# Kernel tuning notes

Measured on AMD Instinct MI355X. Metric: run time of the kernel, lower is better.

The kernel has to match this reference:

```python
import jax, jax.numpy as jnp
import numpy as np
from jax import lax
from jax.scipy.special import logsumexp

B, T, N = 256, 512, 128


def setup_inputs() -> dict:
    key = jax.random.key(0)
    k1, k2, k3 = jax.random.split(key, 3)
    emissions = jax.random.normal(k1, (B, T, N), dtype=jnp.float32)
    tag_ids = jax.random.randint(k2, (B, T), 0, N, dtype=jnp.int64)
    mask = jnp.ones((B, T), dtype=jnp.int32)
    # learned transition matrix (glorot-uniform-ish init)
    limit = float(np.sqrt(6.0 / (N + N)))
    trans = jax.random.uniform(k3, (N, N), minval=-limit, maxval=limit, dtype=jnp.float32)
    return {"emissions": emissions, "tag_ids": tag_ids, "mask": mask, "trans": trans}


def _sequence_score(emissions, tag_ids, maskf, trans):
    # unary: emission score of the gold tag at each valid step
    unary = jnp.take_along_axis(emissions, tag_ids[:, :, None], axis=2)[..., 0]  # [B,T]
    unary = jnp.sum(unary * maskf, axis=1)
    # binary: transition score between consecutive gold tags
    binary = trans[tag_ids[:, :-1], tag_ids[:, 1:]] * maskf[:, 1:]  # [B,T-1]
    return unary + jnp.sum(binary, axis=1)


def _log_norm(emissions, maskf, trans):
    # forward algorithm over time via lax.scan; alpha: [B,N]
    alpha0 = emissions[:, 0]
    em = jnp.swapaxes(emissions, 0, 1)[1:]   # [T-1,B,N]
    mk = jnp.swapaxes(maskf, 0, 1)[1:]       # [T-1,B]

    def step(alpha, xs):
        emit_t, m_t = xs
        new = logsumexp(alpha[:, :, None] + trans[None], axis=1) + emit_t
        alpha = jnp.where(m_t[:, None] > 0, new, alpha)
        return alpha, None

    alpha, _ = lax.scan(step, alpha0, (em, mk))
    return logsumexp(alpha, axis=1)  # [B]


def _viterbi_decode(emissions, maskf, trans):
    alpha0 = emissions[:, 0]
    em = jnp.swapaxes(emissions, 0, 1)[1:]
    mk = jnp.swapaxes(maskf, 0, 1)[1:]
    idx = jnp.arange(N, dtype=jnp.int32)[None]

    def fwd(alpha, xs):
        emit_t, m_t = xs
        scores = alpha[:, :, None] + trans[None]        # [B,N,N]
        bp = jnp.argmax(scores, axis=1).astype(jnp.int32)  # [B,N]
        new = jnp.max(scores, axis=1) + emit_t
        valid = m_t[:, None] > 0
        alpha = jnp.where(valid, new, alpha)
        bp = jnp.where(valid, bp, idx)  # carry same tag through padding
        return alpha, bp

    alpha, bps = lax.scan(fwd, alpha0, (em, mk))  # bps: [T-1,B,N]
    last_tag = jnp.argmax(alpha, axis=1).astype(jnp.int32)  # [B]

    def bwd(tag, bp_t):
        new_tag = jnp.take_along_axis(bp_t, tag[:, None], axis=1)[:, 0]
        return new_tag, new_tag

    _, tags_rev = lax.scan(bwd, last_tag, bps[::-1])  # [T-1,B]
    tags = jnp.concatenate([tags_rev[::-1], last_tag[None]], axis=0)  # [T,B]
    return jnp.swapaxes(tags, 0, 1)  # [B,T]


def reference(emissions, tag_ids, mask, trans):
    maskf = mask.astype(emissions.dtype)
    log_likelihood = _sequence_score(emissions, tag_ids, maskf, trans) - _log_norm(emissions, maskf, trans)
    predict = _viterbi_decode(emissions, maskf, trans)
    return (log_likelihood, trans, predict)
```

## Files before the change

### kernel.cpp

```cpp
#include <hip/hip_runtime.h>
#include <cmath>

#define BB 256
#define TT 512
#define NN 128
#define LN2F 0.6931471805599453f

__device__ __forceinline__ float wave_max64(float v) {
    #pragma unroll
    for (int off = 32; off; off >>= 1) v = fmaxf(v, __shfl_xor(v, off));
    return v;
}
__device__ __forceinline__ float wave_sum64(float v) {
    #pragma unroll
    for (int off = 32; off; off >>= 1) v += __shfl_xor(v, off);
    return v;
}
__device__ __forceinline__ int wave_argmax128(float v0, float v1, int l) {
    float m = fmaxf(v0, v1);
    float wm = wave_max64(m);
    unsigned long long ball = __ballot(m == wm);
    int lane = __ffsll(ball) - 1;
    int idx = (v0 == wm) ? (2 * l) : (2 * l + 1);
    return __shfl(idx, lane);
}

__device__ __forceinline__ int padidx(int i) { return 36 * (i >> 5) + (i & 31); }

__global__ __launch_bounds__(1024, 4) void fwd_kernel(
        const float* __restrict__ em, const int* __restrict__ mask,
        const float* __restrict__ trans, float* __restrict__ outp,
        float* __restrict__ lognorm) {
    const int b = blockIdx.x;
    const int tid = threadIdx.x;
    const int w = tid >> 6;
    const int l = tid & 63;
    const bool isV = (w < 8);
    const int wl = w & 7;
    const int j = (l & 15) + 16 * wl;
    const int q = l >> 4;
    const int i0 = 32 * q;

    float C[32];
    {
        const float* tc = trans + (size_t)i0 * NN + j;
        #pragma unroll
        for (int r = 0; r < 32; ++r) C[r] = tc[(size_t)r * NN];
        if (!isV) {
            #pragma unroll
            for (int r = 0; r < 32; ++r) C[r] = __expf(C[r]);
        }
    }

    __shared__ __align__(16) float apad[2][144];
    __shared__ __align__(16) float spad[2][144];
    __shared__ unsigned char bp_lds[TT * NN];
    __shared__ unsigned char tags_lds[TT];
    __shared__ int msk[TT];
    __shared__ float piv[2];
    __shared__ float sfin[NN];
    __shared__ int kacc_sh;

    if (tid < TT) msk[tid] = mask[b * TT + tid];

    const float* emb = em + (size_t)b * TT * NN;

    float e0 = emb[j];
    float st = 0.f;
    int kacc = 0;
    if (isV) {
        st = e0;
        if (l < 16) apad[0][padidx(j)] = st;
    } else {
        st = __expf(e0);
        if (l < 16) spad[0][padidx(j)] = st;
        if (w == 8 && l == 0) piv[0] = st;
    }
    float e_next = emb[NN + j];
    __syncthreads();

    for (int t = 1; t < TT; ++t) {
        const float e_cur = e_next;
        if (t + 1 < TT) e_next = emb[(size_t)(t + 1) * NN + j];
        const int m = msk[t];
        const int p = (t - 1) & 1, qb = t & 1;

        if (isV) {
            const float4* ap = (const float4*)(apad[p] + 36 * q);
            float m0 = -INFINITY, m1 = -INFINITY, m2 = -INFINITY, m3 = -INFINITY;
            int u0 = 0, u1 = 0, u2 = 0, u3 = 0;
            #pragma unroll
            for (int u = 0; u < 8; ++u) {
                float4 v = ap[u];
                float c0 = v.x + C[4*u+0];
                float c1 = v.y + C[4*u+1];
                float c2 = v.z + C[4*u+2];
                float c3 = v.w + C[4*u+3];
                if (c0 > m0) { m0 = c0; u0 = u; }
                if (c1 > m1) { m1 = c1; u1 = u; }
                if (c2 > m2) { m2 = c2; u2 = u; }
                if (c3 > m3) { m3 = c3; u3 = u; }
            }
            float bv = m0; int bi = i0 + 4 * u0;
            { int id = i0 + 4*u1 + 1; if (m1 > bv || (m1 == bv && id < bi)) { bv = m1; bi = id; } }
            { int id = i0 + 4*u2 + 2; if (m2 > bv || (m2 == bv && id < bi)) { bv = m2; bi = id; } }
            { int id = i0 + 4*u3 + 3; if (m3 > bv || (m3 == bv && id < bi)) { bv = m3; bi = id; } }
            #pragma unroll
            for (int off = 16; off <= 32; off <<= 1) {
                float ov = __shfl_xor(bv, off);
                int oi = __shfl_xor(bi, off);
                if (ov > bv || (ov == bv && oi < bi)) { bv = ov; bi = oi; }
            }
            if (l < 16) {
                float av_new; int bp;
                if (m) { av_new = bv + e_cur; bp = bi; }
                else   { av_new = st;         bp = j;  }
                st = av_new;
                apad[qb][padidx(j)] = av_new;
                bp_lds[t * NN + j] = (unsigned char)bp;
            }
        } else {
            const float pv = piv[p];
            const float4* sp = (const float4*)(spad[p] + 36 * q);
            float d0 = 0, d1 = 0, d2 = 0, d3 = 0;
            #pragma unroll
            for (int u = 0; u < 8; ++u) {
                float4 v = sp[u];
                d0 = fmaf(v.x, C[4*u+0], d0);
                d1 = fmaf(v.y, C[4*u+1], d1);
                d2 = fmaf(v.z, C[4*u+2], d2);
                d3 = fmaf(v.w, C[4*u+3], d3);
            }
            float dot = (d0 + d1) + (d2 + d3);
            dot += __shfl_xor(dot, 16);
            dot += __shfl_xor(dot, 32);
            const int k = (int)(__float_as_uint(pv) >> 23) - 127;
            const float scale = __uint_as_float((unsigned)(127 - k) << 23);
            float s_new;
            if (m) { s_new = dot * scale * __expf(e_cur); kacc += k; }
            else   { s_new = st; }
            st = s_new;
            if (l < 16) {
                spad[qb][padidx(j)] = s_new;
                if (tid == 512 + 0 && false) {}
            }
            if (w == 8 && l == 0) piv[qb] = s_new;
        }
        __syncthreads();
    }

    if (!isV && l < 16) sfin[j] = st;
    if (w == 8 && l == 0) kacc_sh = kacc;
    __syncthreads();

    if (w == 0) {
        float v = sfin[2 * l] + sfin[2 * l + 1];
        v = wave_sum64(v);
        if (l == 0) lognorm[b] = __logf(v) + (float)kacc_sh * LN2F;
    } else if (w == 1) {
        float a0 = apad[(TT - 1) & 1][padidx(2 * l)];
        float a1 = apad[(TT - 1) & 1][padidx(2 * l + 1)];
        int tag = wave_argmax128(a0, a1, l);
        if (l == 0) {
            tags_lds[TT - 1] = (unsigned char)tag;
            for (int t = TT - 1; t >= 1; --t) {
                tag = bp_lds[t * NN + tag];
                tags_lds[t - 1] = (unsigned char)tag;
            }
        }
    }
    __syncthreads();
    if (tid < TT) outp[(size_t)b * TT + tid] = (float)tags_lds[tid];
}

__global__ __launch_bounds__(128, 1) void score_kernel(
        const float* __restrict__ em, const int* __restrict__ tags,
        const int* __restrict__ mask, const float* __restrict__ trans,
        const float* __restrict__ lognorm, float* __restrict__ out_ll) {
    const int b = blockIdx.x;
    const int tid = threadIdx.x;
    float acc = 0.f;
    for (int t = tid; t < TT; t += 128) {
        int tg = tags[b * TT + t];
        float mf = (float)mask[b * TT + t];
        acc += em[((size_t)b * TT + t) * NN + tg] * mf;
        if (t >= 1) {
            int tp = tags[b * TT + t - 1];
            acc += trans[tp * NN + tg] * mf;
        }
    }
    acc = wave_sum64(acc);
    __shared__ float rs[2];
    if ((tid & 63) == 0) rs[tid >> 6] = acc;
    __syncthreads();
    if (tid == 0) out_ll[b] = (rs[0] + rs[1]) - lognorm[b];
}

__global__ void copy_trans_kernel(const float* __restrict__ trans,
                                  float* __restrict__ dst) {
    int i = blockIdx.x * 256 + threadIdx.x;
    if (i < NN * NN) dst[i] = trans[i];
}

extern "C" void kernel_launch(void* const* d_in, const int* in_sizes, int n_in,
                              void* d_out, int out_size, void* d_ws, size_t ws_size,
                              hipStream_t stream) {
    const float* em = (const float*)d_in[0];
    const int* tags = (const int*)d_in[1];
    const int* mask = (const int*)d_in[2];
    const float* trans = (const float*)d_in[3];

    float* out = (float*)d_out;
    float* out_ll = out;
    float* out_trans = out + BB;
    float* out_pred = out + BB + NN * NN;

    float* lognorm = (float*)d_ws;

    hipLaunchKernelGGL(fwd_kernel, dim3(BB), dim3(1024), 0, stream,
                       em, mask, trans, out_pred, lognorm);
    hipLaunchKernelGGL(copy_trans_kernel, dim3(64), dim3(256), 0, stream,
                       trans, out_trans);
    hipLaunchKernelGGL(score_kernel, dim3(BB), dim3(128), 0, stream,
                       em, tags, mask, trans, lognorm, out_ll);
}
```

Baseline: 585.2 us.

## Split Viterbi and forward recurrences into separate 512-thread blocks with parallel backtrace

```diff
diff --git a/kernel.cpp b/kernel.cpp
--- a/kernel.cpp
+++ b/kernel.cpp
@@ -27,17 +27,17 @@
 
 __device__ __forceinline__ int padidx(int i) { return 36 * (i >> 5) + (i & 31); }
 
-__global__ __launch_bounds__(1024, 4) void fwd_kernel(
+__global__ __launch_bounds__(512, 2) void fwd_kernel(
         const float* __restrict__ em, const int* __restrict__ mask,
         const float* __restrict__ trans, float* __restrict__ outp,
         float* __restrict__ lognorm) {
-    const int b = blockIdx.x;
+    const int bi = blockIdx.x;
+    const int b = bi >> 1;
+    const bool isV = (bi & 1) == 0;
     const int tid = threadIdx.x;
     const int w = tid >> 6;
     const int l = tid & 63;
-    const bool isV = (w < 8);
-    const int wl = w & 7;
-    const int j = (l & 15) + 16 * wl;
+    const int j = (l & 15) + 16 * w;
     const int q = l >> 4;
     const int i0 = 32 * q;
 
@@ -52,76 +52,121 @@
         }
     }
 
-    __shared__ __align__(16) float apad[2][144];
-    __shared__ __align__(16) float spad[2][144];
+    __shared__ __align__(16) float stA[144], stB[144];
     __shared__ unsigned char bp_lds[TT * NN];
     __shared__ unsigned char tags_lds[TT];
+    __shared__ unsigned char map_lds[8 * NN];
+    __shared__ int entry_sh[8];
     __shared__ int msk[TT];
     __shared__ float piv[2];
     __shared__ float sfin[NN];
-    __shared__ int kacc_sh;
-
-    if (tid < TT) msk[tid] = mask[b * TT + tid];
+    __shared__ int misc[2];
+
+    msk[tid] = mask[b * TT + tid];
 
     const float* emb = em + (size_t)b * TT * NN;
-
-    float e0 = emb[j];
     float st = 0.f;
     int kacc = 0;
-    if (isV) {
-        st = e0;
-        if (l < 16) apad[0][padidx(j)] = st;
-    } else {
-        st = __expf(e0);
-        if (l < 16) spad[0][padidx(j)] = st;
-        if (w == 8 && l == 0) piv[0] = st;
+    {
+        float a0 = emb[j];
+        if (isV) {
+            st = a0;
+            if (l < 16) stA[padidx(j)] = a0;
+        } else {
+            st = __expf(a0);
+            if (l < 16) stA[padidx(j)] = st;
+            if (tid == 0) piv[0] = st;
+        }
     }
     float e_next = emb[NN + j];
     __syncthreads();
 
-    for (int t = 1; t < TT; ++t) {
-        const float e_cur = e_next;
-        if (t + 1 < TT) e_next = emb[(size_t)(t + 1) * NN + j];
-        const int m = msk[t];
-        const int p = (t - 1) & 1, qb = t & 1;
-
-        if (isV) {
-            const float4* ap = (const float4*)(apad[p] + 36 * q);
+    if (isV) {
+        const float4* apA = (const float4*)(stA + 36 * q);
+        const float4* apB = (const float4*)(stB + 36 * q);
+
+        auto VSTEP = [&](int t, const float4* ap, float* dst) {
+            const float e_cur = e_next;
+            if (t + 1 < TT) e_next = emb[(size_t)(t + 1) * NN + j];
+            const int m = msk[t];
             float m0 = -INFINITY, m1 = -INFINITY, m2 = -INFINITY, m3 = -INFINITY;
             int u0 = 0, u1 = 0, u2 = 0, u3 = 0;
             #pragma unroll
             for (int u = 0; u < 8; ++u) {
                 float4 v = ap[u];
-                float c0 = v.x + C[4*u+0];
-                float c1 = v.y + C[4*u+1];
-                float c2 = v.z + C[4*u+2];
-                float c3 = v.w + C[4*u+3];
-                if (c0 > m0) { m0 = c0; u0 = u; }
-                if (c1 > m1) { m1 = c1; u1 = u; }
-                if (c2 > m2) { m2 = c2; u2 = u; }
-                if (c3 > m3) { m3 = c3; u3 = u; }
-            }
-            float bv = m0; int bi = i0 + 4 * u0;
-            { int id = i0 + 4*u1 + 1; if (m1 > bv || (m1 == bv && id < bi)) { bv = m1; bi = id; } }
-            { int id = i0 + 4*u2 + 2; if (m2 > bv || (m2 == bv && id < bi)) { bv = m2; bi = id; } }
-            { int id = i0 + 4*u3 + 3; if (m3 > bv || (m3 == bv && id < bi)) { bv = m3; bi = id; } }
+                float c0 = v.x + C[4*u+0]; u0 = (c0 > m0) ? u : u0; m0 = fmaxf(m0, c0);
+                float c1 = v.y + C[4*u+1]; u1 = (c1 > m1) ? u : u1; m1 = fmaxf(m1, c1);
+                float c2 = v.z + C[4*u+2]; u2 = (c2 > m2) ? u : u2; m2 = fmaxf(m2, c2);
+                float c3 = v.w + C[4*u+3]; u3 = (c3 > m3) ? u : u3; m3 = fmaxf(m3, c3);
+            }
+            float bv = m0; int bx = i0 + 4 * u0;
+            { int id = i0 + 4*u1 + 1; if (m1 > bv || (m1 == bv && id < bx)) { bv = m1; bx = id; } }
+            { int id = i0 + 4*u2 + 2; if (m2 > bv || (m2 == bv && id < bx)) { bv = m2; bx = id; } }
+            { int id = i0 + 4*u3 + 3; if (m3 > bv || (m3 == bv && id < bx)) { bv = m3; bx = id; } }
             #pragma unroll
             for (int off = 16; off <= 32; off <<= 1) {
                 float ov = __shfl_xor(bv, off);
-                int oi = __shfl_xor(bi, off);
-                if (ov > bv || (ov == bv && oi < bi)) { bv = ov; bi = oi; }
+                int oi = __shfl_xor(bx, off);
+                if (ov > bv || (ov == bv && oi < bx)) { bv = ov; bx = oi; }
             }
             if (l < 16) {
-                float av_new; int bp;
-                if (m) { av_new = bv + e_cur; bp = bi; }
-                else   { av_new = st;         bp = j;  }
-                st = av_new;
-                apad[qb][padidx(j)] = av_new;
+                float an; int bp;
+                if (m) { an = bv + e_cur; bp = bx; }
+                else   { an = st;         bp = j;  }
+                st = an;
+                dst[padidx(j)] = an;
                 bp_lds[t * NN + j] = (unsigned char)bp;
             }
-        } else {
-            const float pv = piv[p];
-            const float4* sp = (const float4*)(spad[p] + 36 * q);
+            __syncthreads();
+        };
+
+        for (int t = 1; t < TT - 1; t += 2) {
+            VSTEP(t, apA, stB);
+            VSTEP(t + 1, apB, stA);
+        }
+        VSTEP(TT - 1, apA, stB);
+
+        if (w == 0) {
+            float a0 = stB[padidx(2 * l)], a1 = stB[padidx(2 * l + 1)];
+            int tg = wave_argmax128(a0, a1, l);
+            if (l == 0) { misc[0] = tg; tags_lds[TT - 1] = (unsigned char)tg; }
+        }
+        const int lo = 64 * w + 1;
+        const int hi = (w == 7) ? (TT - 1) : (64 * w + 64);
+        {
+            int tA = 2 * l, tB = 2 * l + 1;
+            for (int t = hi; t >= lo; --t) {
+                tA = bp_lds[t * NN + tA];
+                tB = bp_lds[t * NN + tB];
+            }
+            map_lds[w * NN + 2 * l]     = (unsigned char)tA;
+            map_lds[w * NN + 2 * l + 1] = (unsigned char)tB;
+        }
+        __syncthreads();
+        if (tid == 0) {
+            int e = misc[0];
+            entry_sh[7] = e;
+            for (int c = 7; c >= 1; --c) { e = map_lds[c * NN + e]; entry_sh[c - 1] = e; }
+        }
+        __syncthreads();
+        if (l == 0) {
+            int tg = entry_sh[w];
+            for (int t = hi; t >= lo; --t) {
+                tg = bp_lds[t * NN + tg];
+                tags_lds[t - 1] = (unsigned char)tg;
+            }
+        }
+        __syncthreads();
+        outp[(size_t)b * TT + tid] = (float)tags_lds[tid];
+    } else {
+        const float4* spA = (const float4*)(stA + 36 * q);
+        const float4* spB = (const float4*)(stB + 36 * q);
+
+        auto LSTEP = [&](int t, const float4* sp, float* dst, int pp, int pq) {
+            const float e_cur = e_next;
+            if (t + 1 < TT) e_next = emb[(size_t)(t + 1) * NN + j];
+            const int m = msk[t];
+            const float pv = piv[pp];
             float d0 = 0, d1 = 0, d2 = 0, d3 = 0;
             #pragma unroll
             for (int u = 0; u < 8; ++u) {
@@ -136,41 +181,32 @@
             dot += __shfl_xor(dot, 32);
             const int k = (int)(__float_as_uint(pv) >> 23) - 127;
             const float scale = __uint_as_float((unsigned)(127 - k) << 23);
-            float s_new;
-            if (m) { s_new = dot * scale * __expf(e_cur); kacc += k; }
-            else   { s_new = st; }
-            st = s_new;
+            float sn;
+            if (m) { sn = dot * scale * __expf(e_cur); kacc += k; }
+            else   { sn = st; }
+            st = sn;
             if (l < 16) {
-                spad[qb][padidx(j)] = s_new;
-                if (tid == 512 + 0 && false) {}
-            }
-            if (w == 8 && l == 0) piv[qb] = s_new;
-        }
-        __syncthreads();
-    }
-
-    if (!isV && l < 16) sfin[j] = st;
-    if (w == 8 && l == 0) kacc_sh = kacc;
-    __syncthreads();
-
-    if (w == 0) {
-        float v = sfin[2 * l] + sfin[2 * l + 1];
-        v = wave_sum64(v);
-        if (l == 0) lognorm[b] = __logf(v) + (float)kacc_sh * LN2F;
-    } else if (w == 1) {
-        float a0 = apad[(TT - 1) & 1][padidx(2 * l)];
-        float a1 = apad[(TT - 1) & 1][padidx(2 * l + 1)];
-        int tag = wave_argmax128(a0, a1, l);
-        if (l == 0) {
-            tags_lds[TT - 1] = (unsigned char)tag;
-            for (int t = TT - 1; t >= 1; --t) {
-                tag = bp_lds[t * NN + tag];
-                tags_lds[t - 1] = (unsigned char)tag;
-            }
-        }
-    }
-    __syncthreads();
-    if (tid < TT) outp[(size_t)b * TT + tid] = (float)tags_lds[tid];
+                dst[padidx(j)] = sn;
+                if (tid == 0) piv[pq] = sn;
+            }
+            __syncthreads();
+        };
+
+        for (int t = 1; t < TT - 1; t += 2) {
+            LSTEP(t, spA, stB, 0, 1);
+            LSTEP(t + 1, spB, stA, 1, 0);
+        }
+        LSTEP(TT - 1, spA, stB, 0, 1);
+
+        if (l < 16) sfin[j] = st;
+        if (tid == 0) misc[1] = kacc;
+        __syncthreads();
+        if (w == 0) {
+            float v = sfin[2 * l] + sfin[2 * l + 1];
+            v = wave_sum64(v);
+            if (l == 0) lognorm[b] = __logf(v) + (float)misc[1] * LN2F;
+        }
+    }
 }
 
 __global__ __launch_bounds__(128, 1) void score_kernel(
@@ -217,7 +253,7 @@
 
     float* lognorm = (float*)d_ws;
 
-    hipLaunchKernelGGL(fwd_kernel, dim3(BB), dim3(1024), 0, stream,
+    hipLaunchKernelGGL(fwd_kernel, dim3(2 * BB), dim3(512), 0, stream,
                        em, mask, trans, out_pred, lognorm);
     hipLaunchKernelGGL(copy_trans_kernel, dim3(64), dim3(256), 0, stream,
                        trans, out_trans);
```

Result: slower. 682.8 us (+16.7%).
